# Performance work log

Measured on AMD Instinct MI355X. Metric: run time of the kernel, lower is better.

The kernel has to match this reference:

```python
import jax, jax.numpy as jnp
import numpy as np
import math

S, B, D, H = 2048, 2, 1024, 16
DK = D // H

def setup_inputs() -> dict:
    key = jax.random.key(0)
    ks = jax.random.split(key, 32)
    f = lambda k, shape, s=1.0: jax.random.normal(k, shape, dtype=jnp.float32) * s
    inp = {
        'qx': f(ks[0], (S, B, D)),
        'kx': f(ks[1], (S, B, D)),
        'vx': f(ks[2], (S, B, D)),
        'qc': f(ks[3], (S, B, D)),
        'kc': f(ks[4], (S, B, D)),
    }
    w = 1.0 / math.sqrt(D)
    names = ['qx_lin', 'kx_lin', 'vx_lin', 'qc_lin', 'kc_lin', 'out_lin']
    for i, n in enumerate(names):
        inp['W_' + n] = f(ks[5 + 2 * i], (D, D), w)
        inp['b_' + n] = f(ks[6 + 2 * i], (D,), w)
    vnames = ['Vqx', 'Vqc', 'Vkx', 'Vkc']
    for i, n in enumerate(vnames):
        inp['W_' + n] = f(ks[17 + 2 * i], (D, 1), w)
        inp['b_' + n] = f(ks[18 + 2 * i], (1,), w)
    return inp

def _forward(qx, kx, vx, qc, kc,
             W_qx_lin, b_qx_lin, W_kx_lin, b_kx_lin, W_vx_lin, b_vx_lin,
             W_qc_lin, b_qc_lin, W_kc_lin, b_kc_lin, W_out_lin, b_out_lin,
             W_Vqx, b_Vqx, W_Vqc, b_Vqc, W_Vkx, b_Vkx, W_Vkc, b_Vkc):
    # [S,B,D] -> [B,S,D]
    qx = jnp.swapaxes(qx, 0, 1)
    kx = jnp.swapaxes(kx, 0, 1)
    vx = jnp.swapaxes(vx, 0, 1)
    qc = jnp.swapaxes(qc, 0, 1)
    kc = jnp.swapaxes(kc, 0, 1)
    bs = qx.shape[0]

    qx = qx @ W_qx_lin + b_qx_lin
    kx = kx @ W_kx_lin + b_kx_lin
    v = vx @ W_vx_lin + b_vx_lin
    qc = qc @ W_qc_lin + b_qc_lin
    kc = kc @ W_kc_lin + b_kc_lin

    lam_q = jax.nn.sigmoid((qx @ W_Vqx + b_Vqx) + (qc @ W_Vqc + b_Vqc))  # [B,S,1]
    lam_k = jax.nn.sigmoid((kx @ W_Vkx + b_Vkx) + (kc @ W_Vkc + b_Vkc))
    q = (1.0 - lam_q) * qx + lam_q * qc
    k = (1.0 - lam_k) * kx + lam_k * kc

    # [B,S,D] -> [B,H,S,dk]
    q = q.reshape(bs, -1, H, DK).transpose(0, 2, 1, 3)
    k = k.reshape(bs, -1, H, DK).transpose(0, 2, 1, 3)
    v = v.reshape(bs, -1, H, DK).transpose(0, 2, 1, 3)

    scores = jnp.einsum('bhqd,bhkd->bhqk', q, k) / math.sqrt(DK)
    attn = jax.nn.softmax(scores, axis=-1)  # dropout is identity in eval
    ctx = jnp.einsum('bhqk,bhkd->bhqd', attn, v)

    concat = ctx.transpose(0, 2, 1, 3).reshape(bs, -1, D)
    out = concat @ W_out_lin + b_out_lin
    return jnp.swapaxes(out, 0, 1)  # back to [S,B,D]

def reference(qx, kx, vx, qc, kc,
              W_qx_lin, b_qx_lin, W_kx_lin, b_kx_lin, W_vx_lin, b_vx_lin,
              W_qc_lin, b_qc_lin, W_kc_lin, b_kc_lin, W_out_lin, b_out_lin,
              W_Vqx, b_Vqx, W_Vqc, b_Vqc, W_Vkx, b_Vkx, W_Vkc, b_Vkc):
    return _forward(qx, kx, vx, qc, kc,
                    W_qx_lin, b_qx_lin, W_kx_lin, b_kx_lin, W_vx_lin, b_vx_lin,
                    W_qc_lin, b_qc_lin, W_kc_lin, b_kc_lin, W_out_lin, b_out_lin,
                    W_Vqx, b_Vqx, W_Vqc, b_Vqc, W_Vkx, b_Vkx, W_Vkc, b_Vkc)
```

## Files before the change

kernel.cpp:

```cpp
#include <hip/hip_runtime.h>
#include <math.h>

typedef unsigned short u16;
typedef __attribute__((ext_vector_type(8))) short short8;
typedef __attribute__((ext_vector_type(4))) float floatx4;
typedef __attribute__((ext_vector_type(4))) unsigned short ushort4v;
typedef __attribute__((ext_vector_type(2))) unsigned int uint2v;

__device__ __forceinline__ float bf2f(u16 x) {
    union { unsigned int u; float f; } v; v.u = ((unsigned int)x) << 16; return v.f;
}
__device__ __forceinline__ u16 f2bf(float f) {
    union { float f; unsigned int u; } v; v.f = f;
    unsigned int r = v.u + 0x7fffu + ((v.u >> 16) & 1u);
    return (u16)(r >> 16);
}
__device__ __forceinline__ unsigned int pk2bf(float a, float b) {
#if __has_builtin(__builtin_amdgcn_cvt_pk_bf16_f32)
    auto r = __builtin_amdgcn_cvt_pk_bf16_f32(a, b);
    union { decltype(r) v; unsigned int u; } cv; cv.v = r; return cv.u;
#else
    return (unsigned int)f2bf(a) | ((unsigned int)f2bf(b) << 16);
#endif
}

struct WFuseJobs { const float* W[4]; const float* wv[4]; const float* bl[4];
                   float* out[4]; float* bdot; };

__global__ __launch_bounds__(256) void wfuse(WFuseJobs wf) {
    const int z = blockIdx.y;
    const float* W = wf.W[z];
    const float* wv = wf.wv[z];
    float* out = wf.out[z];
    const int t = threadIdx.x;
    const int lane = t & 63, w = t >> 6;
#pragma unroll
    for (int i = 0; i < 4; i++) {
        const int row = blockIdx.x * 16 + w * 4 + i;
        const float* Wr = W + (size_t)row * 1024 + lane * 16;
        const float* vr = wv + lane * 16;
        float p = 0.f;
#pragma unroll
        for (int c = 0; c < 4; c++) {
            const floatx4 a = *(const floatx4*)(Wr + c * 4);
            const floatx4 b = *(const floatx4*)(vr + c * 4);
            p += a[0] * b[0] + a[1] * b[1] + a[2] * b[2] + a[3] * b[3];
        }
#pragma unroll
        for (int m = 1; m <= 32; m <<= 1) p += __shfl_xor(p, m);
        if (lane == 0) out[row] = p;
    }
    if (blockIdx.x == 0) {
        const floatx4 bb = *(const floatx4*)(wf.bl[z] + t * 4);
        const floatx4 vv = *(const floatx4*)(wv + t * 4);
        float p = bb[0] * vv[0] + bb[1] * vv[1] + bb[2] * vv[2] + bb[3] * vv[3];
#pragma unroll
        for (int m = 1; m <= 32; m <<= 1) p += __shfl_xor(p, m);
        __shared__ float red[4];
        if ((t & 63) == 0) red[t >> 6] = p;
        __syncthreads();
        if (t == 0) wf.bdot[z] = red[0] + red[1] + red[2] + red[3];
    }
}

struct GCJobs {
    const float* xa[3]; const float* xc[3];
    const float* w1[3]; const float* w2[3];
    const float* bdot;
    const float* sA[3]; const float* sB[3];
    float* lamout[3];
    u16* dst[3];
};

__global__ __launch_bounds__(256) void gatecast(GCJobs gj) {
    const int z = blockIdx.y;
    const int row = blockIdx.x;
    const int t = threadIdx.x;
    const size_t off = (size_t)row * 1024 + t * 4;
    const floatx4 a = *(const floatx4*)(gj.xa[z] + off);

    if (z == 2) {
        ushort4v o;
        const unsigned int lo = pk2bf(a[0], a[1]);
        const unsigned int hi = pk2bf(a[2], a[3]);
        o[0] = (u16)(lo & 0xffff); o[1] = (u16)(lo >> 16);
        o[2] = (u16)(hi & 0xffff); o[3] = (u16)(hi >> 16);
        *(ushort4v*)(gj.dst[2] + (size_t)row * 1024 + t * 4) = o;
        return;
    }

    const floatx4 c  = *(const floatx4*)(gj.xc[z] + off);
    const floatx4 w1 = *(const floatx4*)(gj.w1[z] + t * 4);
    const floatx4 w2 = *(const floatx4*)(gj.w2[z] + t * 4);
    float p = 0.f;
#pragma unroll
    for (int j = 0; j < 4; j++) p += a[j] * w1[j] + c[j] * w2[j];
#pragma unroll
    for (int m = 1; m <= 32; m <<= 1) p += __shfl_xor(p, m);
    __shared__ float red[4];
    if ((t & 63) == 0) red[t >> 6] = p;
    __syncthreads();
    const float x = red[0] + red[1] + red[2] + red[3]
                  + gj.bdot[2 * z] + gj.bdot[2 * z + 1]
                  + gj.sA[z][0] + gj.sB[z][0];
    const float lam = 1.f / (1.f + exp2f(-x * 1.44269504f));
    if (t == 0) gj.lamout[z][row] = lam;
    const float oml = 1.f - lam;

    u16* d = gj.dst[z] + (size_t)row * 2048 + t * 4;
    ushort4v o1, o2;
    {
        const unsigned int lo = pk2bf(oml * a[0], oml * a[1]);
        const unsigned int hi = pk2bf(oml * a[2], oml * a[3]);
        o1[0] = (u16)(lo & 0xffff); o1[1] = (u16)(lo >> 16);
        o1[2] = (u16)(hi & 0xffff); o1[3] = (u16)(hi >> 16);
    }
    {
        const unsigned int lo = pk2bf(lam * c[0], lam * c[1]);
        const unsigned int hi = pk2bf(lam * c[2], lam * c[3]);
        o2[0] = (u16)(lo & 0xffff); o2[1] = (u16)(lo >> 16);
        o2[2] = (u16)(hi & 0xffff); o2[3] = (u16)(hi >> 16);
    }
    *(ushort4v*)d = o1;
    *(ushort4v*)(d + 1024) = o2;
}

struct WTJobs { const float* src[6]; u16* dst[6]; int stride[6]; int koff[6]; };

__global__ __launch_bounds__(256) void wtrans(WTJobs wj) {
    __shared__ float tile[32][33];
    const int z = blockIdx.z;
    const float* W = wj.src[z];
    u16* Wt = wj.dst[z];
    const int stride = wj.stride[z], koff = wj.koff[z];
    const int n0 = blockIdx.x * 32, k0 = blockIdx.y * 32;
    const int tx = threadIdx.x & 31, ty = threadIdx.x >> 5;
#pragma unroll
    for (int i = 0; i < 4; i++)
        tile[ty + i * 8][tx] = W[(size_t)(k0 + ty + i * 8) * 1024 + n0 + tx];
    __syncthreads();
#pragma unroll
    for (int i = 0; i < 4; i++)
        Wt[(size_t)(n0 + ty + i * 8) * stride + koff + k0 + tx] = f2bf(tile[tx][ty + i * 8]);
}

__global__ __launch_bounds__(256) void vtrans(const u16* __restrict__ V,
                                              u16* __restrict__ Vtg) {
    __shared__ u16 tile[32][34];
    const int bh = blockIdx.z, b = bh >> 4, h = bh & 15;
    const int base = b * 1024 + h * 64;
    const int s0 = blockIdx.x * 32, d0 = blockIdx.y * 32;
    const int tx = threadIdx.x & 31, ty = threadIdx.x >> 5;
#pragma unroll
    for (int i = 0; i < 4; i++)
        tile[ty + i * 8][tx] = V[(size_t)(s0 + ty + i * 8) * 2048 + base + d0 + tx];
    __syncthreads();
#pragma unroll
    for (int i = 0; i < 4; i++)
        Vtg[((size_t)bh * 64 + d0 + ty + i * 8) * 2048 + s0 + tx] = tile[tx][ty + i * 8];
}

struct PJob {
    const u16* A; const u16* Bt; int K;
    const float* biasA; const float* biasC; const float* lam; u16* out;
};
struct PJobs { PJob j[3]; };

__global__ __launch_bounds__(256, 3) void projall(PJobs jobs) {
    __shared__ u16 As[128 * 32];
    __shared__ u16 Bs[128 * 32];
    const PJob jb = jobs.j[blockIdx.z];
    const int K = jb.K;
    const int m0 = blockIdx.y * 128;
    const int n0 = blockIdx.x * 128;
    const int t = threadIdx.x;
    const int lane = t & 63;
    const int wid = t >> 6;
    const int wm = wid >> 1, wn = wid & 1;
    const int qd = lane >> 4, lm = lane & 15;

    const floatx4 zero4 = {0.f, 0.f, 0.f, 0.f};
    floatx4 acc[4][4];
#pragma unroll
    for (int i = 0; i < 4; i++)
#pragma unroll
        for (int j2 = 0; j2 < 4; j2++) acc[i][j2] = zero4;

    const int srow = t >> 1, colb = (t & 1) * 16;
    const u16* Ap = jb.A + (size_t)(m0 + srow) * K + colb;
    const u16* Bp = jb.Bt + (size_t)(n0 + srow) * K + colb;
    u16* awr = &As[srow * 32 + colb];
    u16* bwr = &Bs[srow * 32 + colb];

    short8 pa0 = *(const short8*)Ap;
    short8 pa1 = *(const short8*)(Ap + 8);
    short8 pb0 = *(const short8*)Bp;
    short8 pb1 = *(const short8*)(Bp + 8);

    for (int k0 = 0; k0 < K; k0 += 32) {
        __syncthreads();
        *(short8*)awr       = pa0;
        *(short8*)(awr + 8) = pa1;
        *(short8*)bwr       = pb0;
        *(short8*)(bwr + 8) = pb1;
        if (k0 + 32 < K) {
            Ap += 32; Bp += 32;
            pa0 = *(const short8*)Ap;
            pa1 = *(const short8*)(Ap + 8);
            pb0 = *(const short8*)Bp;
            pb1 = *(const short8*)(Bp + 8);
        }
        __syncthreads();

        short8 af[4], bfg[4];
#pragma unroll
        for (int i = 0; i < 4; i++) {
            af[i]  = *(const short8*)&As[(wm * 64 + i * 16 + lm) * 32 + qd * 8];
            bfg[i] = *(const short8*)&Bs[(wn * 64 + i * 16 + lm) * 32 + qd * 8];
        }
#pragma unroll
        for (int i = 0; i < 4; i++)
#pragma unroll
            for (int j2 = 0; j2 < 4; j2++)
                acc[i][j2] = __builtin_amdgcn_mfma_f32_16x16x32_bf16(af[i], bfg[j2], acc[i][j2], 0, 0, 0);
    }

#pragma unroll
    for (int i = 0; i < 4; i++) {
        const int mb = m0 + wm * 64 + i * 16 + qd * 4;
        float lamv[4];
        if (jb.lam) {
#pragma unroll
            for (int r = 0; r < 4; r++) lamv[r] = jb.lam[mb + r];
        }
#pragma unroll
        for (int j2 = 0; j2 < 4; j2++) {
            const int col = n0 + wn * 64 + j2 * 16 + lm;
            const float bA = jb.biasA[col];
            if (jb.lam) {
                const float dB = jb.biasC[col] - bA;
#pragma unroll
                for (int r = 0; r < 4; r++)
                    jb.out[(size_t)(mb + r) * 1024 + col] = f2bf(acc[i][j2][r] + bA + lamv[r] * dB);
            } else {
#pragma unroll
                for (int r = 0; r < 4; r++)
                    jb.out[(size_t)(mb + r) * 1024 + col] = f2bf(acc[i][j2][r] + bA);
            }
        }
    }
}

__global__ __launch_bounds__(256, 4) void gemm64(const u16* __restrict__ A,
                                                 const u16* __restrict__ Bt,
                                                 const float* __restrict__ bias,
                                                 float* __restrict__ C) {
    __shared__ u16 As[64 * 32];
    __shared__ u16 Bs[128 * 32];
    const int K = 1024;
    const int m0 = blockIdx.y * 64;
    const int n0 = blockIdx.x * 128;
    const int t = threadIdx.x;
    const int lane = t & 63;
    const int wid = t >> 6;
    const int wm = wid >> 1, wn = wid & 1;
    const int qd = lane >> 4, lm = lane & 15;

    const floatx4 zero4 = {0.f, 0.f, 0.f, 0.f};
    floatx4 acc[2][4];
#pragma unroll
    for (int i = 0; i < 2; i++)
#pragma unroll
        for (int j2 = 0; j2 < 4; j2++) acc[i][j2] = zero4;

    const int ar = t >> 2, ac_ = (t & 3) * 8;
    const int br = t >> 1, bc_ = (t & 1) * 16;
    const u16* Ap = A + (size_t)(m0 + ar) * K + ac_;
    const u16* Bp = Bt + (size_t)(n0 + br) * K + bc_;
    u16* awr = &As[ar * 32 + ac_];
    u16* bwr = &Bs[br * 32 + bc_];

    short8 pa0, pb0, pb1;
    pa0 = *(const short8*)Ap;
    pb0 = *(const short8*)Bp; pb1 = *(const short8*)(Bp + 8);

    for (int k0 = 0; k0 < K; k0 += 32) {
        __syncthreads();
        *(short8*)awr = pa0;
        *(short8*)bwr = pb0;
        *(short8*)(bwr + 8) = pb1;
        if (k0 + 32 < K) {
            Ap += 32; Bp += 32;
            pa0 = *(const short8*)Ap;
            pb0 = *(const short8*)Bp; pb1 = *(const short8*)(Bp + 8);
        }
        __syncthreads();

        short8 af[2], bfg[4];
#pragma unroll
        for (int i = 0; i < 2; i++)
            af[i] = *(const short8*)&As[(wm * 32 + i * 16 + lm) * 32 + qd * 8];
#pragma unroll
        for (int j2 = 0; j2 < 4; j2++)
            bfg[j2] = *(const short8*)&Bs[(wn * 64 + j2 * 16 + lm) * 32 + qd * 8];
#pragma unroll
        for (int i = 0; i < 2; i++)
#pragma unroll
            for (int j2 = 0; j2 < 4; j2++)
                acc[i][j2] = __builtin_amdgcn_mfma_f32_16x16x32_bf16(af[i], bfg[j2], acc[i][j2], 0, 0, 0);
    }

#pragma unroll
    for (int i = 0; i < 2; i++) {
        const int mb = m0 + wm * 32 + i * 16 + qd * 4;
#pragma unroll
        for (int j2 = 0; j2 < 4; j2++) {
            const int col = n0 + wn * 64 + j2 * 16 + lm;
            const float bv = bias[col];
#pragma unroll
            for (int r = 0; r < 4; r++)
                C[(size_t)(mb + r) * 1024 + col] = acc[i][j2][r] + bv;
        }
    }
}

__global__ __launch_bounds__(256, 2) void attn4(
    const u16* __restrict__ Q, const u16* __restrict__ Kk,
    const u16* __restrict__ Vtg, float* __restrict__ ctxp,
    float* __restrict__ lp) {
    __shared__ u16 Ks[64 * 72];
    __shared__ u16 Vs[64 * 72];
    __shared__ u16 Ps[4 * 64 * 72];

    const int bh = blockIdx.y, b = bh >> 4, h = bh & 15;
    const int sp = blockIdx.z;
    const int base = b * 1024 + h * 64;
    const int t = threadIdx.x, lane = t & 63, w = t >> 6;
    const int qd = lane >> 4, lm = lane & 15;
    const int q0w = blockIdx.x * 256 + w * 64;

    short8 qf[4][2];
#pragma unroll
    for (int qh = 0; qh < 4; qh++) {
        const u16* qr = Q + (size_t)(q0w + qh * 16 + lm) * 2048 + base;
#pragma unroll
        for (int c = 0; c < 2; c++)
            qf[qh][c] = *(const short8*)(qr + c * 32 + qd * 8);
    }

    const floatx4 zero4 = {0.f, 0.f, 0.f, 0.f};
    floatx4 ctx[4][4];
#pragma unroll
    for (int qh = 0; qh < 4; qh++)
#pragma unroll
        for (int g = 0; g < 4; g++) ctx[qh][g] = zero4;
    float lpart[4] = {0.f, 0.f, 0.f, 0.f};

    u16* Pw = &Ps[w * 64 * 72];
    const float C = 0.18033688011112042f;

    const int sr = t >> 3, sc = (t & 7) * 8;
    const u16* ksrc = Kk + (size_t)(sp * 1024 + sr) * 2048 + base + sc;
    const u16* vsrc = Vtg + ((size_t)bh * 64 + sr) * 2048 + sp * 1024 + sc;
    u16* kdst0 = &Ks[sr * 72 + sc];
    u16* kdst1 = &Ks[(sr + 32) * 72 + sc];
    u16* vdst0 = &Vs[sr * 72 + sc];
    u16* vdst1 = &Vs[(sr + 32) * 72 + sc];

    short8 ka0 = *(const short8*)ksrc;
    short8 ka1 = *(const short8*)(ksrc + (size_t)32 * 2048);
    short8 va0 = *(const short8*)vsrc;
    short8 va1 = *(const short8*)(vsrc + (size_t)32 * 2048);

    for (int kt = 0; kt < 16; kt++) {
        __syncthreads();
        *(short8*)kdst0 = ka0;
        *(short8*)kdst1 = ka1;
        *(short8*)vdst0 = va0;
        *(short8*)vdst1 = va1;
        __syncthreads();
        if (kt < 15) {
            ksrc += (size_t)64 * 2048;
            vsrc += 64;
            ka0 = *(const short8*)ksrc;
            ka1 = *(const short8*)(ksrc + (size_t)32 * 2048);
            va0 = *(const short8*)vsrc;
            va1 = *(const short8*)(vsrc + (size_t)32 * 2048);
        }

#pragma unroll
        for (int g = 0; g < 4; g++) {
            const short8 kf0 = *(const short8*)&Ks[(g * 16 + lm) * 72 + qd * 8];
            const short8 kf1 = *(const short8*)&Ks[(g * 16 + lm) * 72 + 32 + qd * 8];
#pragma unroll
            for (int qh = 0; qh < 4; qh++) {
                floatx4 st = zero4;
                st = __builtin_amdgcn_mfma_f32_16x16x32_bf16(kf0, qf[qh][0], st, 0, 0, 0);
                st = __builtin_amdgcn_mfma_f32_16x16x32_bf16(kf1, qf[qh][1], st, 0, 0, 0);
                const float p0 = exp2f(st[0] * C);
                const float p1 = exp2f(st[1] * C);
                const float p2 = exp2f(st[2] * C);
                const float p3 = exp2f(st[3] * C);
                lpart[qh] += (p0 + p1) + (p2 + p3);
                uint2v pw;
                pw[0] = pk2bf(p0, p1);
                pw[1] = pk2bf(p2, p3);
                *(uint2v*)&Pw[(qh * 16 + lm) * 72 + g * 16 + qd * 4] = pw;
            }
        }

        short8 pa[4][2];
#pragma unroll
        for (int qh = 0; qh < 4; qh++)
#pragma unroll
            for (int c = 0; c < 2; c++)
                pa[qh][c] = *(const short8*)&Pw[(qh * 16 + lm) * 72 + c * 32 + qd * 8];
#pragma unroll
        for (int g = 0; g < 4; g++) {
            const short8 vb0 = *(const short8*)&Vs[(g * 16 + lm) * 72 + qd * 8];
            const short8 vb1 = *(const short8*)&Vs[(g * 16 + lm) * 72 + 32 + qd * 8];
#pragma unroll
            for (int qh = 0; qh < 4; qh++) {
                ctx[qh][g] = __builtin_amdgcn_mfma_f32_16x16x32_bf16(pa[qh][0], vb0, ctx[qh][g], 0, 0, 0);
                ctx[qh][g] = __builtin_amdgcn_mfma_f32_16x16x32_bf16(pa[qh][1], vb1, ctx[qh][g], 0, 0, 0);
            }
        }
    }

    float* cbase = ctxp + (size_t)sp * 4194304;
#pragma unroll
    for (int qh = 0; qh < 4; qh++) {
        float l = lpart[qh];
        l += __shfl_xor(l, 16);
        l += __shfl_xor(l, 32);
        if (lane < 16)
            lp[(size_t)sp * 65536 + bh * 2048 + q0w + qh * 16 + lane] = l;
#pragma unroll
        for (int r = 0; r < 4; r++) {
            const int srow = q0w + qh * 16 + qd * 4 + r;
            float* orow = cbase + (size_t)srow * 2048 + base;
#pragma unroll
            for (int g = 0; g < 4; g++)
                orow[g * 16 + lm] = ctx[qh][g][r];
        }
    }
}

__global__ __launch_bounds__(256) void merge(const float* __restrict__ ctxp,
                                             const float* __restrict__ lp,
                                             u16* __restrict__ out) {
    const size_t idx = ((size_t)blockIdx.x * 256 + threadIdx.x) * 4;
    const floatx4 a = *(const floatx4*)(ctxp + idx);
    const floatx4 c = *(const floatx4*)(ctxp + 4194304 + idx);
    const int srow = (int)(idx >> 11);
    const int rem = (int)(idx & 2047);
    const int bh = rem >> 6;
    const float l = lp[bh * 2048 + srow] + lp[65536 + bh * 2048 + srow];
    const float inv = 1.0f / l;
    ushort4v o;
    const unsigned int lo = pk2bf((a[0] + c[0]) * inv, (a[1] + c[1]) * inv);
    const unsigned int hi = pk2bf((a[2] + c[2]) * inv, (a[3] + c[3]) * inv);
    o[0] = (u16)(lo & 0xffff); o[1] = (u16)(lo >> 16);
    o[2] = (u16)(hi & 0xffff); o[3] = (u16)(hi >> 16);
    *(ushort4v*)(out + idx) = o;
}

extern "C" void kernel_launch(void* const* d_in, const int* in_sizes, int n_in,
                              void* d_out, int out_size, void* d_ws, size_t ws_size,
                              hipStream_t stream) {
    const float* qx = (const float*)d_in[0];
    const float* kx = (const float*)d_in[1];
    const float* vx = (const float*)d_in[2];
    const float* qc = (const float*)d_in[3];
    const float* kc = (const float*)d_in[4];
    const float* W_qx = (const float*)d_in[5];   const float* b_qx = (const float*)d_in[6];
    const float* W_kx = (const float*)d_in[7];   const float* b_kx = (const float*)d_in[8];
    const float* W_vx = (const float*)d_in[9];   const float* b_vx = (const float*)d_in[10];
    const float* W_qc = (const float*)d_in[11];  const float* b_qc = (const float*)d_in[12];
    const float* W_kc = (const float*)d_in[13];  const float* b_kc = (const float*)d_in[14];
    const float* W_out = (const float*)d_in[15]; const float* b_out = (const float*)d_in[16];
    const float* W_Vqx = (const float*)d_in[17]; const float* b_Vqx = (const float*)d_in[18];
    const float* W_Vqc = (const float*)d_in[19]; const float* b_Vqc = (const float*)d_in[20];
    const float* W_Vkx = (const float*)d_in[21]; const float* b_Vkx = (const float*)d_in[22];
    const float* W_Vkc = (const float*)d_in[23]; const float* b_Vkc = (const float*)d_in[24];

    char* ws = (char*)d_ws;
    const size_t MB = 1048576;
    u16* Aq  = (u16*)ws;
    u16* Ak  = (u16*)(ws + 16 * MB);
    u16* Av  = (u16*)(ws + 32 * MB);
    u16* Wtq = (u16*)(ws + 40 * MB);
    u16* Wtk = (u16*)(ws + 44 * MB);
    u16* Wtv = (u16*)(ws + 48 * MB);
    u16* Wto = (u16*)(ws + 50 * MB);
    u16* Pv    = (u16*)(ws + 52 * MB);
    u16* qg    = (u16*)(ws + 60 * MB);
    u16* kg    = (u16*)(ws + 68 * MB);
    u16* ctxbf = (u16*)(ws + 76 * MB);
    float* wfused = (float*)(ws + 84 * MB);
    float* bdot   = (float*)(ws + 84 * MB + 16384);
    float* lam    = (float*)(ws + 84 * MB + 16384 + 256);
    float* l_part = (float*)(ws + 84 * MB + 16384 + 256 + 32768);
    float* ctxp = (float*)ws;
    u16* Vtg    = (u16*)(ws + 32 * MB);

    WFuseJobs wf;
    wf.W[0] = W_qx; wf.wv[0] = W_Vqx; wf.bl[0] = b_qx; wf.out[0] = wfused;
    wf.W[1] = W_qc; wf.wv[1] = W_Vqc; wf.bl[1] = b_qc; wf.out[1] = wfused + 1024;
    wf.W[2] = W_kx; wf.wv[2] = W_Vkx; wf.bl[2] = b_kx; wf.out[2] = wfused + 2048;
    wf.W[3] = W_kc; wf.wv[3] = W_Vkc; wf.bl[3] = b_kc; wf.out[3] = wfused + 3072;
    wf.bdot = bdot;
    wfuse<<<dim3(64, 4), 256, 0, stream>>>(wf);

    GCJobs gj;
    gj.xa[0] = qx; gj.xc[0] = qc; gj.w1[0] = wfused;        gj.w2[0] = wfused + 1024;
    gj.sA[0] = b_Vqx; gj.sB[0] = b_Vqc; gj.lamout[0] = lam;        gj.dst[0] = Aq;
    gj.xa[1] = kx; gj.xc[1] = kc; gj.w1[1] = wfused + 2048; gj.w2[1] = wfused + 3072;
    gj.sA[1] = b_Vkx; gj.sB[1] = b_Vkc; gj.lamout[1] = lam + 4096; gj.dst[1] = Ak;
    gj.xa[2] = vx; gj.xc[2] = nullptr; gj.w1[2] = nullptr; gj.w2[2] = nullptr;
    gj.sA[2] = nullptr; gj.sB[2] = nullptr; gj.lamout[2] = nullptr; gj.dst[2] = Av;
    gj.bdot = bdot;
    gatecast<<<dim3(4096, 3), 256, 0, stream>>>(gj);

    WTJobs wj;
    wj.src[0] = W_qx; wj.dst[0] = Wtq; wj.stride[0] = 2048; wj.koff[0] = 0;
    wj.src[1] = W_qc; wj.dst[1] = Wtq; wj.stride[1] = 2048; wj.koff[1] = 1024;
    wj.src[2] = W_kx; wj.dst[2] = Wtk; wj.stride[2] = 2048; wj.koff[2] = 0;
    wj.src[3] = W_kc; wj.dst[3] = Wtk; wj.stride[3] = 2048; wj.koff[3] = 1024;
    wj.src[4] = W_vx; wj.dst[4] = Wtv; wj.stride[4] = 1024; wj.koff[4] = 0;
    wj.src[5] = W_out; wj.dst[5] = Wto; wj.stride[5] = 1024; wj.koff[5] = 0;
    wtrans<<<dim3(32, 32, 6), 256, 0, stream>>>(wj);

    PJobs pj;
    pj.j[0].A = Aq; pj.j[0].Bt = Wtq; pj.j[0].K = 2048;
    pj.j[0].biasA = b_qx; pj.j[0].biasC = b_qc; pj.j[0].lam = lam;        pj.j[0].out = qg;
    pj.j[1].A = Ak; pj.j[1].Bt = Wtk; pj.j[1].K = 2048;
    pj.j[1].biasA = b_kx; pj.j[1].biasC = b_kc; pj.j[1].lam = lam + 4096; pj.j[1].out = kg;
    pj.j[2].A = Av; pj.j[2].Bt = Wtv; pj.j[2].K = 1024;
    pj.j[2].biasA = b_vx; pj.j[2].biasC = nullptr; pj.j[2].lam = nullptr; pj.j[2].out = Pv;
    projall<<<dim3(8, 32, 3), 256, 0, stream>>>(pj);

    vtrans<<<dim3(64, 2, 32), 256, 0, stream>>>(Pv, Vtg);

    attn4<<<dim3(8, 32, 2), 256, 0, stream>>>(qg, kg, Vtg, ctxp, l_part);

    merge<<<4096, 256, 0, stream>>>(ctxp, l_part, ctxbf);

    gemm64<<<dim3(8, 64), 256, 0, stream>>>(ctxbf, Wto, b_out, (float*)d_out);
}
```

Measured before the change: 353.7 us.

## Rewrite attention kernel with async LDS double-buffering and register-resident P

Replaces attn4 with attn5. Each wave now handles 32 queries instead of 64, so the grid doubles and occupancy is raised to 4 blocks per CU. K/V tiles are staged with global_load_lds into XOR-swizzled, double-buffered shared memory. The P matrix is now rearranged in registers with permlane swaps instead of a round trip through LDS, and the PV MFMAs run at raised priority. Block IDs are remapped to spread work across XCDs. The aims are to hide global-load latency, cut LDS traffic and bank conflicts, and overlap softmax with MFMA work, at the cost of reloading the K/V tiles twice as often per query.

```diff
diff --git a/kernel.cpp b/kernel.cpp
--- a/kernel.cpp
+++ b/kernel.cpp
@@ -22,6 +22,41 @@
 #else
     return (unsigned int)f2bf(a) | ((unsigned int)f2bf(b) << 16);
 #endif
+}
+
+__device__ __forceinline__ void swap32(unsigned int& x0, unsigned int& x1, int lane) {
+#if __has_builtin(__builtin_amdgcn_permlane32_swap)
+    (void)lane;
+    auto r = __builtin_amdgcn_permlane32_swap((int)x0, (int)x1, false, false);
+    x0 = (unsigned int)r[0]; x1 = (unsigned int)r[1];
+#else
+    const bool hi = (lane & 32) != 0;
+    const unsigned int s = hi ? x0 : x1;
+    const unsigned int rr = (unsigned int)__shfl_xor((int)s, 32, 64);
+    const unsigned int n0 = hi ? rr : x0;
+    const unsigned int n1 = hi ? x1 : rr;
+    x0 = n0; x1 = n1;
+#endif
+}
+__device__ __forceinline__ void swap16(unsigned int& x0, unsigned int& x1, int lane) {
+#if __has_builtin(__builtin_amdgcn_permlane16_swap)
+    (void)lane;
+    auto r = __builtin_amdgcn_permlane16_swap((int)x0, (int)x1, false, false);
+    x0 = (unsigned int)r[0]; x1 = (unsigned int)r[1];
+#else
+    const bool hi = (lane & 16) != 0;
+    const unsigned int s = hi ? x0 : x1;
+    const unsigned int rr = (unsigned int)__shfl_xor((int)s, 16, 64);
+    const unsigned int n0 = hi ? rr : x0;
+    const unsigned int n1 = hi ? x1 : rr;
+    x0 = n0; x1 = n1;
+#endif
+}
+
+__device__ __forceinline__ void g2l16(const u16* g, u16* l) {
+    __builtin_amdgcn_global_load_lds(
+        (const __attribute__((address_space(1))) void*)g,
+        (__attribute__((address_space(3))) void*)l, 16, 0, 0);
 }
 
 struct WFuseJobs { const float* W[4]; const float* wv[4]; const float* bl[4];
@@ -324,112 +359,124 @@
     }
 }
 
-__global__ __launch_bounds__(256, 2) void attn4(
+__global__ __launch_bounds__(256, 4) void attn5(
     const u16* __restrict__ Q, const u16* __restrict__ Kk,
     const u16* __restrict__ Vtg, float* __restrict__ ctxp,
     float* __restrict__ lp) {
-    __shared__ u16 Ks[64 * 72];
-    __shared__ u16 Vs[64 * 72];
-    __shared__ u16 Ps[4 * 64 * 72];
-
-    const int bh = blockIdx.y, b = bh >> 4, h = bh & 15;
-    const int sp = blockIdx.z;
-    const int base = b * 1024 + h * 64;
+    __shared__ __align__(16) u16 SB[16384];
+
+    const int bid = blockIdx.x + 16 * (blockIdx.y + 32 * blockIdx.z);
+    const int sw = (bid & 7) * 128 + (bid >> 3);
+    const int qt = sw & 15;
+    const int bh = (sw >> 4) & 31;
+    const int sp = sw >> 9;
+    const int b = bh >> 4, h = bh & 15;
+    const int hb = b * 1024 + h * 64;
+
     const int t = threadIdx.x, lane = t & 63, w = t >> 6;
     const int qd = lane >> 4, lm = lane & 15;
-    const int q0w = blockIdx.x * 256 + w * 64;
-
-    short8 qf[4][2];
-#pragma unroll
-    for (int qh = 0; qh < 4; qh++) {
-        const u16* qr = Q + (size_t)(q0w + qh * 16 + lm) * 2048 + base;
+    const int q0w = qt * 128 + w * 32;
+
+    short8 qf[2][2];
+#pragma unroll
+    for (int qh = 0; qh < 2; qh++) {
+        const u16* qr = Q + (size_t)(q0w + qh * 16 + lm) * 2048 + hb;
 #pragma unroll
         for (int c = 0; c < 2; c++)
             qf[qh][c] = *(const short8*)(qr + c * 32 + qd * 8);
     }
 
     const floatx4 zero4 = {0.f, 0.f, 0.f, 0.f};
-    floatx4 ctx[4][4];
-#pragma unroll
-    for (int qh = 0; qh < 4; qh++)
+    floatx4 ctx[2][4];
+#pragma unroll
+    for (int qh = 0; qh < 2; qh++)
 #pragma unroll
         for (int g = 0; g < 4; g++) ctx[qh][g] = zero4;
-    float lpart[4] = {0.f, 0.f, 0.f, 0.f};
-
-    u16* Pw = &Ps[w * 64 * 72];
+    float lpart[2] = {0.f, 0.f};
+
+    const int rl = lane >> 3;
+    const int cuz = (lane & 7) ^ rl;
+    const u16* kp = Kk + (size_t)(sp * 1024 + w * 16 + rl) * 2048 + hb + cuz * 8;
+    const u16* vp = Vtg + ((size_t)bh * 64 + w * 16 + rl) * 2048 + sp * 1024 + cuz * 8;
+    u16* kd = &SB[(w * 16) * 64];
+    u16* vd = &SB[4096 + (w * 16) * 64];
+
+    const int rdA = lm * 64 + ((qd ^ (lm & 7)) << 3);
+    const int rdB = rdA ^ 32;
+
     const float C = 0.18033688011112042f;
 
-    const int sr = t >> 3, sc = (t & 7) * 8;
-    const u16* ksrc = Kk + (size_t)(sp * 1024 + sr) * 2048 + base + sc;
-    const u16* vsrc = Vtg + ((size_t)bh * 64 + sr) * 2048 + sp * 1024 + sc;
-    u16* kdst0 = &Ks[sr * 72 + sc];
-    u16* kdst1 = &Ks[(sr + 32) * 72 + sc];
-    u16* vdst0 = &Vs[sr * 72 + sc];
-    u16* vdst1 = &Vs[(sr + 32) * 72 + sc];
-
-    short8 ka0 = *(const short8*)ksrc;
-    short8 ka1 = *(const short8*)(ksrc + (size_t)32 * 2048);
-    short8 va0 = *(const short8*)vsrc;
-    short8 va1 = *(const short8*)(vsrc + (size_t)32 * 2048);
-
-    for (int kt = 0; kt < 16; kt++) {
-        __syncthreads();
-        *(short8*)kdst0 = ka0;
-        *(short8*)kdst1 = ka1;
-        *(short8*)vdst0 = va0;
-        *(short8*)vdst1 = va1;
-        __syncthreads();
-        if (kt < 15) {
-            ksrc += (size_t)64 * 2048;
-            vsrc += 64;
-            ka0 = *(const short8*)ksrc;
-            ka1 = *(const short8*)(ksrc + (size_t)32 * 2048);
-            va0 = *(const short8*)vsrc;
-            va1 = *(const short8*)(vsrc + (size_t)32 * 2048);
-        }
-
-#pragma unroll
-        for (int g = 0; g < 4; g++) {
-            const short8 kf0 = *(const short8*)&Ks[(g * 16 + lm) * 72 + qd * 8];
-            const short8 kf1 = *(const short8*)&Ks[(g * 16 + lm) * 72 + 32 + qd * 8];
-#pragma unroll
-            for (int qh = 0; qh < 4; qh++) {
-                floatx4 st = zero4;
-                st = __builtin_amdgcn_mfma_f32_16x16x32_bf16(kf0, qf[qh][0], st, 0, 0, 0);
-                st = __builtin_amdgcn_mfma_f32_16x16x32_bf16(kf1, qf[qh][1], st, 0, 0, 0);
-                const float p0 = exp2f(st[0] * C);
-                const float p1 = exp2f(st[1] * C);
-                const float p2 = exp2f(st[2] * C);
-                const float p3 = exp2f(st[3] * C);
-                lpart[qh] += (p0 + p1) + (p2 + p3);
-                uint2v pw;
-                pw[0] = pk2bf(p0, p1);
-                pw[1] = pk2bf(p2, p3);
-                *(uint2v*)&Pw[(qh * 16 + lm) * 72 + g * 16 + qd * 4] = pw;
-            }
-        }
-
-        short8 pa[4][2];
-#pragma unroll
-        for (int qh = 0; qh < 4; qh++)
-#pragma unroll
-            for (int c = 0; c < 2; c++)
-                pa[qh][c] = *(const short8*)&Pw[(qh * 16 + lm) * 72 + c * 32 + qd * 8];
-#pragma unroll
-        for (int g = 0; g < 4; g++) {
-            const short8 vb0 = *(const short8*)&Vs[(g * 16 + lm) * 72 + qd * 8];
-            const short8 vb1 = *(const short8*)&Vs[(g * 16 + lm) * 72 + 32 + qd * 8];
-#pragma unroll
-            for (int qh = 0; qh < 4; qh++) {
-                ctx[qh][g] = __builtin_amdgcn_mfma_f32_16x16x32_bf16(pa[qh][0], vb0, ctx[qh][g], 0, 0, 0);
-                ctx[qh][g] = __builtin_amdgcn_mfma_f32_16x16x32_bf16(pa[qh][1], vb1, ctx[qh][g], 0, 0, 0);
-            }
-        }
-    }
+#define STAGE(BUF) do {                                             \
+        g2l16(kp,            kd + (BUF) * 8192);                    \
+        g2l16(kp + 8 * 2048, kd + (BUF) * 8192 + 8 * 64);           \
+        g2l16(vp,            vd + (BUF) * 8192);                    \
+        g2l16(vp + 8 * 2048, vd + (BUF) * 8192 + 8 * 64);           \
+        kp += 64 * 2048; vp += 64;                                  \
+    } while (0)
+
+#define COMPUTE(BUF) do {                                                          \
+        short8 pa[2][2];                                                           \
+        _Pragma("unroll")                                                          \
+        for (int gp = 0; gp < 2; gp++) {                                           \
+            unsigned int pw[2][2][2];                                              \
+            _Pragma("unroll")                                                      \
+            for (int g0 = 0; g0 < 2; g0++) {                                       \
+                const int g = gp * 2 + g0;                                         \
+                const short8 kf0 = *(const short8*)&SB[(BUF) * 8192 + g * 1024 + rdA]; \
+                const short8 kf1 = *(const short8*)&SB[(BUF) * 8192 + g * 1024 + rdB]; \
+                _Pragma("unroll")                                                  \
+                for (int qh = 0; qh < 2; qh++) {                                   \
+                    floatx4 st = zero4;                                            \
+                    st = __builtin_amdgcn_mfma_f32_16x16x32_bf16(kf0, qf[qh][0], st, 0, 0, 0); \
+                    st = __builtin_amdgcn_mfma_f32_16x16x32_bf16(kf1, qf[qh][1], st, 0, 0, 0); \
+                    const float e0 = exp2f(st[0] * C), e1 = exp2f(st[1] * C);      \
+                    const float e2 = exp2f(st[2] * C), e3 = exp2f(st[3] * C);      \
+                    lpart[qh] += (e0 + e1) + (e2 + e3);                            \
+                    pw[qh][g0][0] = pk2bf(e0, e1);                                 \
+                    pw[qh][g0][1] = pk2bf(e2, e3);                                 \
+                }                                                                  \
+            }                                                                      \
+            _Pragma("unroll")                                                      \
+            for (int qh = 0; qh < 2; qh++) {                                       \
+                unsigned int a0 = pw[qh][0][0], b0 = pw[qh][1][0];                 \
+                unsigned int a1 = pw[qh][0][1], b1 = pw[qh][1][1];                 \
+                swap32(a0, b0, lane); swap32(a1, b1, lane);                        \
+                swap16(a0, b0, lane); swap16(a1, b1, lane);                        \
+                union { unsigned int u[4]; short8 s; } cv;                         \
+                cv.u[0] = a0; cv.u[1] = a1; cv.u[2] = b0; cv.u[3] = b1;            \
+                pa[qh][gp] = cv.s;                                                 \
+            }                                                                      \
+        }                                                                          \
+        __builtin_amdgcn_s_setprio(1);                                             \
+        _Pragma("unroll")                                                          \
+        for (int g = 0; g < 4; g++) {                                              \
+            const short8 vb0 = *(const short8*)&SB[(BUF) * 8192 + 4096 + g * 1024 + rdA]; \
+            const short8 vb1 = *(const short8*)&SB[(BUF) * 8192 + 4096 + g * 1024 + rdB]; \
+            _Pragma("unroll")                                                      \
+            for (int qh = 0; qh < 2; qh++) {                                       \
+                ctx[qh][g] = __builtin_amdgcn_mfma_f32_16x16x32_bf16(pa[qh][0], vb0, ctx[qh][g], 0, 0, 0); \
+                ctx[qh][g] = __builtin_amdgcn_mfma_f32_16x16x32_bf16(pa[qh][1], vb1, ctx[qh][g], 0, 0, 0); \
+            }                                                                      \
+        }                                                                          \
+        __builtin_amdgcn_s_setprio(0);                                             \
+    } while (0)
+
+    STAGE(0);
+#pragma unroll 1
+    for (int it = 0; it < 8; it++) {
+        __syncthreads();
+        STAGE(1);
+        COMPUTE(0);
+        __syncthreads();
+        if (it < 7) STAGE(0);
+        COMPUTE(1);
+    }
+#undef STAGE
+#undef COMPUTE
 
     float* cbase = ctxp + (size_t)sp * 4194304;
 #pragma unroll
-    for (int qh = 0; qh < 4; qh++) {
+    for (int qh = 0; qh < 2; qh++) {
         float l = lpart[qh];
         l += __shfl_xor(l, 16);
         l += __shfl_xor(l, 32);
@@ -438,7 +485,7 @@
 #pragma unroll
         for (int r = 0; r < 4; r++) {
             const int srow = q0w + qh * 16 + qd * 4 + r;
-            float* orow = cbase + (size_t)srow * 2048 + base;
+            float* orow = cbase + (size_t)srow * 2048 + hb;
 #pragma unroll
             for (int g = 0; g < 4; g++)
                 orow[g * 16 + lm] = ctx[qh][g][r];
@@ -542,7 +589,7 @@
 
     vtrans<<<dim3(64, 2, 32), 256, 0, stream>>>(Pv, Vtg);
 
-    attn4<<<dim3(8, 32, 2), 256, 0, stream>>>(qg, kg, Vtg, ctxp, l_part);
+    attn5<<<dim3(16, 32, 2), 256, 0, stream>>>(qg, kg, Vtg, ctxp, l_part);
 
     merge<<<4096, 256, 0, stream>>>(ctxp, l_part, ctxbf);
 
```

After: 343.7 us. 2.8% less time.
